# Kernel tuning notes

Measured on AMD Instinct MI355X. Metric: run time of the kernel, lower is better.

The kernel has to match this reference:

```python
import jax, jax.numpy as jnp
import numpy as np

B, T, E = 2, 2048, 2048
H, NOPE, ROPE, VD, KVR, DR = 16, 64, 32, 64, 256, 2
QKD = NOPE + ROPE  # 96
LOWR = KVR // 4    # hypernet low_rank=4 -> 64


def _rope_angles(position, dim):
    # freqs_cis angles: pos * 10000^(-2i/dim), matching torch rotary with theta=10000
    inv = jnp.exp(jnp.arange(0, dim, 2, dtype=jnp.float32) * (-jnp.log(jnp.float32(10000.0)) / dim))
    return position.astype(jnp.float32)[..., None] * inv  # (1, T, dim//2)


def _apply_rotary(x, ang):
    # x: (B,T,H,D); pairs are consecutive elements (view_as_complex semantics)
    x2 = x.reshape(x.shape[:-1] + (-1, 2))
    c = jnp.cos(ang)[:, :, None, :]
    s = jnp.sin(ang)[:, :, None, :]
    xr, xi = x2[..., 0], x2[..., 1]
    return jnp.stack([xr * c - xi * s, xr * s + xi * c], axis=-1).reshape(x.shape)


def _layernorm(x, g, b, eps=1e-5):
    m = jnp.mean(x, axis=-1, keepdims=True)
    v = jnp.var(x, axis=-1, keepdims=True)
    return (x - m) * jax.lax.rsqrt(v + eps) * g + b


def _sinusoid_pe(t, d):
    pos = jnp.arange(t, dtype=jnp.float32)[:, None]
    div = jnp.exp(jnp.arange(0, d, 2, dtype=jnp.float32) * (-jnp.log(jnp.float32(10000.0)) / d))
    pe = jnp.zeros((t, d), dtype=jnp.float32)
    pe = pe.at[:, 0::2].set(jnp.sin(pos * div)).at[:, 1::2].set(jnp.cos(pos * div))
    return pe


def setup_inputs() -> dict:
    key = jax.random.key(0)
    ks = jax.random.split(key, 16)
    sd = 0.02
    return {
        "query": jax.random.normal(ks[0], (B, T, E), jnp.float32),
        "key": jax.random.normal(ks[1], (B, T, E), jnp.float32),
        "value": jax.random.normal(ks[2], (B, T, E), jnp.float32),
        "position": jnp.arange(T, dtype=jnp.int32)[None, :],
        # weights stored transposed for right-multiply (x @ W)
        "wq": jax.random.normal(ks[3], (E, H * QKD), jnp.float32) * sd,
        "wkv_a": jax.random.normal(ks[4], (E, KVR + ROPE), jnp.float32) * sd,
        "kv_gamma": jnp.ones((KVR,), jnp.float32),
        "kv_beta": jnp.zeros((KVR,), jnp.float32),
        # torch layout (H*(NOPE+VD), KVR) kept for faithful view(H,-1,KVR) absorb
        "wkv_b": jax.random.normal(ks[5], (H * (NOPE + VD), KVR), jnp.float32) * sd,
        "wo": jax.random.normal(ks[6], (H * VD, E), jnp.float32) * sd,
        "fc_c_w": jax.random.normal(ks[7], (KVR, LOWR), jnp.float32) * sd,
        "fc_c_b": jnp.zeros((LOWR,), jnp.float32),
        "fc_p_w": jax.random.normal(ks[8], (KVR, LOWR), jnp.float32) * sd,
        "fc_p_b": jnp.zeros((LOWR,), jnp.float32),
    }


def reference(query, key, value, position, wq, wkv_a, kv_gamma, kv_beta, wkv_b, wo,
              fc_c_w, fc_c_b, fc_p_w, fc_p_b):
    bsz, seqlen, _ = query.shape
    # queries: low-rank-free path (q_lora_rank=0)
    q = (query @ wq).reshape(bsz, seqlen, H, QKD)
    q_nope, q_pe = q[..., :NOPE], q[..., NOPE:]
    ang = _rope_angles(position, ROPE)  # (1, T, ROPE//2)
    q_pe = _apply_rotary(q_pe, ang[:, -seqlen:])
    # key/value latent projection
    kv_all = key @ wkv_a  # (B, T, KVR+ROPE)
    kv, k_pe = kv_all[..., :KVR], kv_all[..., KVR:]
    k_pe = _apply_rotary(k_pe[:, :, None, :], ang)[:, :, 0, :]  # (B, T, ROPE)
    kv_norm = _layernorm(kv, kv_gamma, kv_beta)  # (B, T, KVR)
    # hypernetwork temporal downsampling weights (train path, T_input=kv_norm)
    t = -(-seqlen // DR)
    C = jnp.repeat(_sinusoid_pe(t, KVR), DR, axis=0)[:seqlen]  # (T, KVR)
    C2 = C @ fc_c_w + fc_c_b           # (T, LOWR)
    P2 = kv_norm @ fc_p_w + fc_p_b     # (B, T, LOWR)
    W = jax.nn.sigmoid(jnp.einsum('tc,bsc->bts', C2, P2))  # (B, T, T)
    idx = jnp.arange(seqlen)
    chunk = idx // DR
    # chunk mask: cumulative within-chunk causal accumulation
    zero_mask = ((chunk[:, None] == chunk[None, :]) & (idx[None, :] <= idx[:, None])).astype(query.dtype)
    kv_t = jnp.einsum('bts,bsc->btc', W * zero_mask, kv_norm)  # (B, T, KVR)
    # stride-aware causal mask: attend completed chunk-end slots + own in-progress slot
    allowed = (idx[None, :] == idx[:, None]) | ((idx[None, :] < idx[:, None]) & (((idx[None, :] + 1) % DR) == 0))
    attn_mask = jnp.where(allowed, jnp.float32(0.0), jnp.float32(-1e30))
    # absorbed MLA attention
    wb = wkv_b.reshape(H, NOPE + VD, KVR)
    q_abs = jnp.einsum('bshd,hdc->bshc', q_nope, wb[:, :NOPE])  # (B, S, H, KVR)
    scores = (jnp.einsum('bshc,btc->bsht', q_abs, kv_t)
              + jnp.einsum('bshr,btr->bsht', q_pe, k_pe)) * (QKD ** -0.5)
    scores = scores + attn_mask[None, :, None, :]
    attn = jax.nn.softmax(scores, axis=-1)
    x = jnp.einsum('bsht,btc->bshc', attn, kv_t)
    x = jnp.einsum('bshc,hdc->bshd', x, wb[:, NOPE:])  # (B, S, H, VD)
    return x.reshape(bsz, seqlen, H * VD) @ wo
```

## Files before the change

kernel.cpp:

```cpp
#include <hip/hip_runtime.h>
#include <stddef.h>

typedef unsigned short u16;
typedef unsigned short u16x8 __attribute__((ext_vector_type(8)));
typedef short s16x8 __attribute__((ext_vector_type(8)));
typedef float f32x4 __attribute__((ext_vector_type(4)));

#define B_ 2
#define T_ 2048
#define E_ 2048
#define H_ 16

__device__ inline float us2f(u16 u){
  unsigned int i = ((unsigned int)u) << 16;
  return __builtin_bit_cast(float, i);
}
__device__ inline u16 f2us(float f){
  unsigned int x = __builtin_bit_cast(unsigned int, f);
  unsigned int r = (x + 0x7fffu + ((x >> 16) & 1u)) >> 16;
  return (u16)r;
}
__device__ inline f32x4 mfma32(s16x8 a, s16x8 b, f32x4 c){
  return __builtin_amdgcn_mfma_f32_16x16x32_bf16(a, b, c, 0, 0, 0);
}
__device__ inline s16x8 ld8(const u16* p){
  return __builtin_bit_cast(s16x8, *(const u16x8*)p);
}
__device__ inline void gload_lds16(const u16* g, u16* l){
  __builtin_amdgcn_global_load_lds(
      (const __attribute__((address_space(1))) unsigned int*)(g),
      (__attribute__((address_space(3))) unsigned int*)(l), 16, 0, 0);
}

__global__ __launch_bounds__(256) void prep_weights(
    const float* __restrict__ wq, const float* __restrict__ wkva,
    const float* __restrict__ wo, const float* __restrict__ wkvb,
    u16* __restrict__ wqT, u16* __restrict__ wkvaT, u16* __restrict__ woT,
    u16* __restrict__ wkvbB)
{
  __shared__ float tile[32][33];
  const int bid = blockIdx.x;
  const int tid = threadIdx.x;
  if (bid < 5696) {
    const float* in; u16* out; int R, C, bx, by;
    if (bid < 3072)      { in = wq;   out = wqT;   R = 2048; C = 1536; bx = bid % 48;          by = bid / 48; }
    else if (bid < 3648) { in = wkva; out = wkvaT; R = 2048; C = 288;  bx = (bid-3072) % 9;    by = (bid-3072) / 9; }
    else                 { in = wo;   out = woT;   R = 1024; C = 2048; bx = (bid-3648) % 64;   by = (bid-3648) / 64; }
    int tx = tid & 31, ty = tid >> 5;
    int c0 = bx * 32, r0 = by * 32;
    for (int i = ty; i < 32; i += 8){
      int r = r0 + i, c = c0 + tx;
      tile[i][tx] = (r < R && c < C) ? in[(size_t)r * C + c] : 0.f;
    }
    __syncthreads();
    for (int i = ty; i < 32; i += 8){
      int c = c0 + i, r = r0 + tx;
      if (c < C && r < R) out[(size_t)c * R + r] = f2us(tile[tx][i]);
    }
  } else {
    int i = (bid - 5696) * 1024 + tid * 4;
    f32x4 v = *(const f32x4*)(wkvb + i);
    wkvbB[i]   = f2us(v[0]); wkvbB[i+1] = f2us(v[1]);
    wkvbB[i+2] = f2us(v[2]); wkvbB[i+3] = f2us(v[3]);
  }
}

__global__ __launch_bounds__(256) void cvt2_f32_bf16(const float* __restrict__ a,
    const float* __restrict__ b, u16* __restrict__ oa, u16* __restrict__ ob, int n_each)
{
  int idx = (blockIdx.x * 256 + threadIdx.x) * 4;
  const float* in; u16* out; int i;
  if (idx < n_each){ in = a; out = oa; i = idx; }
  else             { in = b; out = ob; i = idx - n_each; }
  if (i + 3 < n_each){
    f32x4 v = *(const f32x4*)(in + i);
    out[i]   = f2us(v[0]); out[i+1] = f2us(v[1]);
    out[i+2] = f2us(v[2]); out[i+3] = f2us(v[3]);
  }
}

template<int A_F32, int OUT_F32>
__global__ __launch_bounds__(256) void gemm_bt(const void* __restrict__ Ap,
    const u16* __restrict__ Bt, void* __restrict__ Cp, int M, int N, int K)
{
  __shared__ __align__(16) u16 As[64][40];
  __shared__ __align__(16) u16 Bs[64][40];
  const int tid  = threadIdx.x;
  const int lane = tid & 63;
  const int wid  = tid >> 6;
  const int quad = lane >> 4;
  const int col  = lane & 15;
  const int bm = blockIdx.y * 64;
  const int bn = blockIdx.x * 64;
  const int lr = tid >> 2;
  const int lc = (tid & 3) * 8;
  const int waveM = wid >> 1, waveN = wid & 1;

  f32x4 acc[2][2];
  for (int i = 0; i < 2; ++i)
    for (int j = 0; j < 2; ++j)
      acc[i][j] = (f32x4){0.f, 0.f, 0.f, 0.f};

  const u16x8 zero8 = {0,0,0,0,0,0,0,0};
  const bool bok = (bn + lr) < N;
  const u16*   arow16 = (const u16*)Ap   + (size_t)(bm + lr) * K + lc;
  const float* arow32 = (const float*)Ap + (size_t)(bm + lr) * K + lc;
  const u16* brow = Bt + (size_t)(bn + lr) * K + lc;

  for (int kk = 0; kk < K; kk += 32) {
    u16x8 av;
    if (A_F32) {
      f32x4 a0 = *(const f32x4*)(arow32 + kk);
      f32x4 a1 = *(const f32x4*)(arow32 + kk + 4);
      av[0]=f2us(a0[0]); av[1]=f2us(a0[1]); av[2]=f2us(a0[2]); av[3]=f2us(a0[3]);
      av[4]=f2us(a1[0]); av[5]=f2us(a1[1]); av[6]=f2us(a1[2]); av[7]=f2us(a1[3]);
    } else {
      av = *(const u16x8*)(arow16 + kk);
    }
    u16x8 bv = bok ? *(const u16x8*)(brow + kk) : zero8;
    __syncthreads();
    *(u16x8*)&As[lr][lc] = av;
    *(u16x8*)&Bs[lr][lc] = bv;
    __syncthreads();
    s16x8 af0 = ld8(&As[waveM*32 + col][quad*8]);
    s16x8 af1 = ld8(&As[waveM*32 + 16 + col][quad*8]);
    s16x8 bf0 = ld8(&Bs[waveN*32 + col][quad*8]);
    s16x8 bf1 = ld8(&Bs[waveN*32 + 16 + col][quad*8]);
    acc[0][0] = mfma32(af0, bf0, acc[0][0]);
    acc[0][1] = mfma32(af0, bf1, acc[0][1]);
    acc[1][0] = mfma32(af1, bf0, acc[1][0]);
    acc[1][1] = mfma32(af1, bf1, acc[1][1]);
  }
  for (int am = 0; am < 2; ++am)
    for (int bnn = 0; bnn < 2; ++bnn)
      for (int i = 0; i < 4; ++i) {
        int r = bm + waveM*32 + am*16 + quad*4 + i;
        int c = bn + waveN*32 + bnn*16 + col;
        if (c < N){
          if (OUT_F32) ((float*)Cp)[(size_t)r * N + c] = acc[am][bnn][i];
          else         ((u16*)Cp)[(size_t)r * N + c]   = f2us(acc[am][bnn][i]);
        }
      }
}

template<int OUT_F32>
__global__ __launch_bounds__(256) void gemm128(const u16* __restrict__ A,
    const u16* __restrict__ Bt, void* __restrict__ Cp, int M, int N, int K, int gx)
{
  __shared__ __align__(16) u16 As[128 * 32];
  __shared__ __align__(16) u16 Bs[128 * 32];
  const int lin = blockIdx.x;
  const int cpx = gridDim.x >> 3;
  const int swz = (lin & 7) * cpx + (lin >> 3);
  const int bxi = swz % gx;
  const int byi = swz / gx;
  const int tid  = threadIdx.x;
  const int lane = tid & 63;
  const int wid  = tid >> 6;
  const int quad = lane >> 4;
  const int col  = lane & 15;
  const int bm = byi * 128;
  const int bn = bxi * 128;
  const int waveM = wid >> 1, waveN = wid & 1;

  const int srow = wid * 16 + (lane >> 2);
  const int scol = (lane & 3) * 8;
  const u16* ga = A  + (size_t)(bm + srow) * K + scol;
  const u16* gb = Bt + (size_t)(bn + srow) * K + scol;
  const size_t rowskip = (size_t)64 * K;
  u16* lAs0 = &As[wid * 512];
  u16* lAs1 = &As[wid * 512 + 2048];
  u16* lBs0 = &Bs[wid * 512];
  u16* lBs1 = &Bs[wid * 512 + 2048];

  f32x4 acc[4][4] = {};

  for (int kk = 0; kk < K; kk += 32) {
    __syncthreads();
    gload_lds16(ga + kk,           lAs0);
    gload_lds16(ga + rowskip + kk, lAs1);
    gload_lds16(gb + kk,           lBs0);
    gload_lds16(gb + rowskip + kk, lBs1);
    __syncthreads();
    s16x8 af[4], bf[4];
#pragma unroll
    for (int i = 0; i < 4; ++i) af[i] = ld8(&As[(waveM*64 + i*16 + col) * 32 + quad*8]);
#pragma unroll
    for (int i = 0; i < 4; ++i) bf[i] = ld8(&Bs[(waveN*64 + i*16 + col) * 32 + quad*8]);
#pragma unroll
    for (int i = 0; i < 4; ++i)
#pragma unroll
      for (int j = 0; j < 4; ++j)
        acc[i][j] = mfma32(af[i], bf[j], acc[i][j]);
  }
#pragma unroll
  for (int i = 0; i < 4; ++i)
#pragma unroll
    for (int j = 0; j < 4; ++j)
#pragma unroll
      for (int r = 0; r < 4; ++r) {
        int row = bm + waveM*64 + i*16 + quad*4 + r;
        int c   = bn + waveN*64 + j*16 + col;
        if (OUT_F32) ((float*)Cp)[(size_t)row * N + c] = acc[i][j][r];
        else         ((u16*)Cp)[(size_t)row * N + c]   = f2us(acc[i][j][r]);
      }
}

__global__ __launch_bounds__(256, 4) void gemm128_sk4(const u16* __restrict__ A,
    const u16* __restrict__ Bt, u16* __restrict__ qp,
    int M, int N, int K, int Klen)
{
  __shared__ __align__(16) u16 As[128 * 32];
  __shared__ __align__(16) u16 Bs[128 * 32];
  const int lin = blockIdx.x;
  const int swz = (lin & 7) * 192 + (lin >> 3);
  const int kh  = swz / 384;
  const int rem = swz % 384;
  const int byi = rem / 12;
  const int bxi = rem % 12;
  const int tid  = threadIdx.x;
  const int lane = tid & 63;
  const int wid  = tid >> 6;
  const int quad = lane >> 4;
  const int col  = lane & 15;
  const int bm = byi * 128;
  const int bn = bxi * 128;
  const int waveM = wid >> 1, waveN = wid & 1;

  const int srow = wid * 16 + (lane >> 2);
  const int scol = (lane & 3) * 8;
  const u16* ga = A  + (size_t)(bm + srow) * K + kh * Klen + scol;
  const u16* gb = Bt + (size_t)(bn + srow) * K + kh * Klen + scol;
  const size_t rowskip = (size_t)64 * K;
  u16* lAs0 = &As[wid * 512];
  u16* lAs1 = &As[wid * 512 + 2048];
  u16* lBs0 = &Bs[wid * 512];
  u16* lBs1 = &Bs[wid * 512 + 2048];
  u16* Cp = qp + (size_t)kh * M * N;

  f32x4 acc[4][4] = {};

  for (int kk = 0; kk < Klen; kk += 32) {
    __syncthreads();
    gload_lds16(ga + kk,           lAs0);
    gload_lds16(ga + rowskip + kk, lAs1);
    gload_lds16(gb + kk,           lBs0);
    gload_lds16(gb + rowskip + kk, lBs1);
    __syncthreads();
    s16x8 af[4], bf[4];
#pragma unroll
    for (int i = 0; i < 4; ++i) af[i] = ld8(&As[(waveM*64 + i*16 + col) * 32 + quad*8]);
#pragma unroll
    for (int i = 0; i < 4; ++i) bf[i] = ld8(&Bs[(waveN*64 + i*16 + col) * 32 + quad*8]);
#pragma unroll
    for (int i = 0; i < 4; ++i)
#pragma unroll
      for (int j = 0; j < 4; ++j)
        acc[i][j] = mfma32(af[i], bf[j], acc[i][j]);
  }
#pragma unroll
  for (int i = 0; i < 4; ++i)
#pragma unroll
    for (int j = 0; j < 4; ++j)
#pragma unroll
      for (int r = 0; r < 4; ++r) {
        int row = bm + waveM*64 + i*16 + quad*4 + r;
        int c   = bn + waveN*64 + j*16 + col;
        Cp[(size_t)row * N + c] = f2us(acc[i][j][r]);
      }
}

__global__ __launch_bounds__(256) void qsplit(const u16* __restrict__ qp,
    const int* __restrict__ pos, u16* __restrict__ qh)
{
  const size_t PS = 4096ull * 1536;
  int idx = blockIdx.x * 256 + threadIdx.x;
  if (idx >= B_*T_*H_*12) return;
  int c    = idx % 12;
  int rest = idx / 12;
  int h    = rest & 15;
  int row  = rest >> 4;
  int t    = row & (T_ - 1);
  int b    = row >> 11;
  size_t off = (size_t)row * 1536 + h * 96 + c * 8;
  u16x8 v0 = *(const u16x8*)(qp + off);
  u16x8 v1 = *(const u16x8*)(qp + PS + off);
  u16x8 v2 = *(const u16x8*)(qp + 2*PS + off);
  u16x8 v3 = *(const u16x8*)(qp + 3*PS + off);
  u16x8 v;
  if (c < 8) {
#pragma unroll
    for (int k = 0; k < 8; ++k)
      v[k] = f2us((us2f(v0[k]) + us2f(v1[k])) + (us2f(v2[k]) + us2f(v3[k])));
  } else {
    int i0 = (c - 8) * 4;
    float pp = (float)pos[t];
#pragma unroll
    for (int k = 0; k < 4; ++k){
      int i = i0 + k;
      float ang = pp * __expf((float)(2*i) * -0.28782313657f);
      float cs = __cosf(ang), sn = __sinf(ang);
      float xr = (us2f(v0[2*k])   + us2f(v1[2*k]))   + (us2f(v2[2*k])   + us2f(v3[2*k]));
      float xi = (us2f(v0[2*k+1]) + us2f(v1[2*k+1])) + (us2f(v2[2*k+1]) + us2f(v3[2*k+1]));
      v[2*k]   = f2us(xr * cs - xi * sn);
      v[2*k+1] = f2us(xr * sn + xi * cs);
    }
  }
  u16* dst = qh + ((size_t)(b * 16 + h) * T_ + t) * 96;
  *(u16x8*)(dst + c * 8) = v;
}

__global__ __launch_bounds__(256) void ln_p2_rope(
    const u16* __restrict__ kvall, const float* __restrict__ gamma,
    const float* __restrict__ beta, const float* __restrict__ fcpw,
    const float* __restrict__ fcpb, const int* __restrict__ pos,
    u16* __restrict__ kvn, float* __restrict__ P2, u16* __restrict__ kpe)
{
  const int row = blockIdx.x;
  if (row >= B_ * T_) return;
  const int tid = threadIdx.x;
  const int lane = tid & 63, wid = tid >> 6;
  __shared__ float kvs[256];
  __shared__ float part[256];
  __shared__ float redS[4], redS2[4];
  const u16* src = kvall + (size_t)row * 288;
  float v = us2f(src[tid]);
  float s1 = v, s2 = v * v;
  for (int off = 1; off < 64; off <<= 1){
    s1 += __shfl_xor(s1, off);
    s2 += __shfl_xor(s2, off);
  }
  if (lane == 0){ redS[wid] = s1; redS2[wid] = s2; }
  __syncthreads();
  float S  = redS[0] + redS[1] + redS[2] + redS[3];
  float Q  = redS2[0] + redS2[1] + redS2[2] + redS2[3];
  float mean = S * (1.f / 256.f);
  float var  = Q * (1.f / 256.f) - mean * mean;
  float rstd = rsqrtf(var + 1e-5f);
  float xn = (v - mean) * rstd * gamma[tid] + beta[tid];
  kvs[tid] = xn;
  kvn[(size_t)row * 256 + tid] = f2us(xn);
  __syncthreads();
  {
    int oc = tid & 63, pp = tid >> 6;
    float acc = 0.f;
#pragma unroll 8
    for (int c = pp * 64; c < pp * 64 + 64; ++c)
      acc += kvs[c] * fcpw[c * 64 + oc];
    part[tid] = acc;
  }
  __syncthreads();
  if (tid < 64) {
    P2[(size_t)row * 64 + tid] = fcpb[tid] + part[tid] + part[64 + tid]
                               + part[128 + tid] + part[192 + tid];
  } else if (tid < 80) {
    int i = tid - 64;
    int t = row & (T_ - 1);
    float ang = (float)pos[t] * __expf((float)(2*i) * -0.28782313657f);
    float c = __cosf(ang), s = __sinf(ang);
    float xr = us2f(src[256 + 2*i]);
    float xi = us2f(src[257 + 2*i]);
    kpe[(size_t)row * 32 + 2*i]     = f2us(xr * c - xi * s);
    kpe[(size_t)row * 32 + 2*i + 1] = f2us(xr * s + xi * c);
  }
}

__global__ __launch_bounds__(256) void c2_kernel(const float* __restrict__ fccw,
    const float* __restrict__ fccb, float* __restrict__ C2)
{
  const int t = blockIdx.x, tid = threadIdx.x;
  __shared__ float pe[256];
  __shared__ float part[256];
  float p = (float)(t >> 1);
  if (tid < 128){
    float div = __expf((float)(2*tid) * -0.03597789207f);
    float a = p * div;
    pe[2*tid]   = __sinf(a);
    pe[2*tid+1] = __cosf(a);
  }
  __syncthreads();
  {
    int oc = tid & 63, pp = tid >> 6;
    float acc = 0.f;
#pragma unroll 8
    for (int c = pp * 64; c < pp * 64 + 64; ++c)
      acc += pe[c] * fccw[c * 64 + oc];
    part[tid] = acc;
  }
  __syncthreads();
  if (tid < 64)
    C2[t * 64 + tid] = fccb[tid] + part[tid] + part[64 + tid]
                     + part[128 + tid] + part[192 + tid];
}

__global__ __launch_bounds__(64) void kvt_kernel(const float* __restrict__ C2,
    const float* __restrict__ P2, const u16* __restrict__ kvn, u16* __restrict__ kvt)
{
  const int row = blockIdx.x;
  if (row >= B_ * T_) return;
  const int lane = threadIdx.x;
  const int t = row & (T_ - 1);
  float c2v = C2[t * 64 + lane];
  float da = c2v * P2[(size_t)row * 64 + lane];
  for (int off = 1; off < 64; off <<= 1) da += __shfl_xor(da, off);
  float wtt = 1.f / (1.f + __expf(-da));
  const bool odd = (t & 1);
  float wts = 0.f;
  if (odd){
    float db = c2v * P2[(size_t)(row - 1) * 64 + lane];
    for (int off = 1; off < 64; off <<= 1) db += __shfl_xor(db, off);
    wts = 1.f / (1.f + __expf(-db));
  }
  for (int c = lane; c < 256; c += 64){
    float val = wtt * us2f(kvn[(size_t)row * 256 + c]);
    if (odd) val += wts * us2f(kvn[(size_t)(row - 1) * 256 + c]);
    kvt[(size_t)row * 256 + c] = f2us(val);
  }
}

__global__ __launch_bounds__(256) void vtkc_kernel(const u16* __restrict__ kvb,
    const u16* __restrict__ kpe, u16* __restrict__ Vt, u16* __restrict__ Kc)
{
  __shared__ __align__(16) u16 tile[64][72];
  const int tid = threadIdx.x;
  if (blockIdx.x < 512) {
    const int bid = blockIdx.x;
    const int jt = bid & 15;
    const int h  = (bid >> 4) & 15;
    const int b  = bid >> 8;
    const int jl = tid >> 2;
    const int dseg = (tid & 3) * 16;
    const int j0 = jt * 64;
    {
      int s_ = 2 * (j0 + jl) + 1;
      const u16* src = kvb + ((size_t)(b * T_ + s_)) * 2048 + h * 128 + 64 + dseg;
      *(u16x8*)&tile[jl][dseg]     = *(const u16x8*)(src);
      *(u16x8*)&tile[jl][dseg + 8] = *(const u16x8*)(src + 8);
    }
    __syncthreads();
    const int dl = tid >> 2;
    const int jseg = (tid & 3) * 16;
    u16* dst = Vt + ((size_t)(b * 16 + h) * 64 + dl) * 1024 + j0 + jseg;
    u16x8 o;
    for (int r = 0; r < 8; ++r) o[r] = tile[jseg + r][dl];
    *(u16x8*)dst = o;
    for (int r = 0; r < 8; ++r) o[r] = tile[jseg + 8 + r][dl];
    *(u16x8*)(dst + 8) = o;
  } else {
    int idx = (blockIdx.x - 512) * 256 + tid;
    int c  = idx % 12;
    int j  = (idx / 12) & 1023;
    int bh = idx / (12 * 1024);
    if (bh >= B_ * H_) return;
    int b = bh >> 4, h = bh & 15;
    int t = 2 * j + 1;
    u16x8 v;
    if (c < 8) v = *(const u16x8*)(kvb + ((size_t)(b * T_ + t)) * 2048 + h * 128 + c * 8);
    else       v = *(const u16x8*)(kpe + ((size_t)(b * T_ + t)) * 32 + (c - 8) * 8);
    int kl = j & 63;
    int cs = (c & 12) | ((c & 3) ^ ((kl >> 1) & 3));
    *(u16x8*)(Kc + ((size_t)bh * 1024 + j) * 96 + cs * 8) = v;
  }
}

__global__ __launch_bounds__(256) void attn_kernel(
    const u16* __restrict__ qh, const u16* __restrict__ kvb,
    const u16* __restrict__ kpe, const u16* __restrict__ Kc,
    const u16* __restrict__ Vt, u16* __restrict__ xout)
{
  __shared__ __align__(16) u16 Ks[64 * 96];
  __shared__ __align__(16) u16 Vs[64][72];
  __shared__ __align__(16) u16 pbufA[4][16 * 72];
  const int tid  = threadIdx.x;
  const int wid  = tid >> 6;
  const int lane = tid & 63;
  const int quad = lane >> 4;
  const int col  = lane & 15;
  const int qt   = 31 - (blockIdx.x >> 5);
  const int bh   = blockIdx.x & 31;
  const int b    = bh >> 4;
  const int h    = bh & 15;
  u16* pbuf = pbufA[wid];
  const float scale = 0.10206207262f;
  const u16* KcH = Kc + (size_t)bh * 1024 * 96;
  const u16* VtH = Vt + (size_t)bh * 64 * 1024;
  const int t0 = qt * 64 + wid * 16;
  const int qo = (quad * 8) ^ (((col >> 1) & 3) << 3);

  s16x8 aq0, aq1, aq2;
  {
    const u16* qrow = qh + ((size_t)bh * T_ + t0 + col) * 96;
    aq0 = ld8(qrow + quad * 8);
    aq1 = ld8(qrow + 32 + quad * 8);
    aq2 = ld8(qrow + 64 + quad * 8);
  }
  float sself;
  {
    const int t = t0 + col;
    const u16* qrow = qh + ((size_t)bh * T_ + t) * 96;
    const u16* ka = kvb + ((size_t)(b * T_ + t)) * 2048 + h * 128;
    const u16* kp = kpe + ((size_t)(b * T_ + t)) * 32;
    float a = 0.f;
#pragma unroll
    for (int c = 0; c < 8; ++c){
      u16x8 qv = *(const u16x8*)(qrow + c * 8);
      u16x8 kv = *(const u16x8*)(ka + c * 8);
#pragma unroll
      for (int jj = 0; jj < 8; ++jj) a += us2f(qv[jj]) * us2f(kv[jj]);
    }
#pragma unroll
    for (int c = 0; c < 4; ++c){
      u16x8 qv = *(const u16x8*)(qrow + 64 + c * 8);
      u16x8 kv = *(const u16x8*)(kp + c * 8);
#pragma unroll
      for (int jj = 0; jj < 8; ++jj) a += us2f(qv[jj]) * us2f(kv[jj]);
    }
    sself = a * scale;
  }
  float es[4], lacc[4];
  f32x4 O[4];
#pragma unroll
  for (int i = 0; i < 4; ++i){
    es[i] = __expf(__shfl(sself, quad * 4 + i));
    lacc[i] = 0.f;
  }
#pragma unroll
  for (int nt = 0; nt < 4; ++nt)
#pragma unroll
    for (int i = 0; i < 4; ++i){
      int t = t0 + quad * 4 + i;
      O[nt][i] = es[i] * us2f(kvb[((size_t)(b * T_ + t)) * 2048 + h * 128 + 64 + nt * 16 + col]);
    }

  const int nb = (qt * 32 + 94) >> 6;
  for (int blk = 0; blk < nb; ++blk) {
    const int jb = blk * 64;
    __syncthreads();
    {
      const u16* gk = KcH + (size_t)jb * 96 + (wid * 3) * 512 + lane * 8;
      u16* lk = &Ks[(wid * 3) * 512];
#pragma unroll
      for (int k = 0; k < 3; ++k)
        gload_lds16(gk + k * 512, lk + k * 512);
      int d = tid >> 2, c4 = tid & 3;
      const u16* gv = VtH + (size_t)d * 1024 + jb + c4 * 16;
      u16* lv = &Vs[d][c4 * 16];
      *(u16x8*)(lv)     = *(const u16x8*)(gv);
      *(u16x8*)(lv + 8) = *(const u16x8*)(gv + 8);
    }
    __syncthreads();
#pragma unroll
    for (int cc = 0; cc < 2; ++cc){
      const u16* k0 = &Ks[(cc * 32 + col) * 96];
      const u16* k1 = k0 + 16 * 96;
      f32x4 s0 = {0,0,0,0}, s1 = {0,0,0,0};
      s0 = mfma32(aq0, ld8(k0 + qo), s0);
      s0 = mfma32(aq1, ld8(k0 + 32 + qo), s0);
      s0 = mfma32(aq2, ld8(k0 + 64 + qo), s0);
      s1 = mfma32(aq0, ld8(k1 + qo), s1);
      s1 = mfma32(aq1, ld8(k1 + 32 + qo), s1);
      s1 = mfma32(aq2, ld8(k1 + 64 + qo), s1);
      int key0 = jb + cc * 32 + col;
#pragma unroll
      for (int i = 0; i < 4; ++i){
        int lim = (t0 + quad * 4 + i) >> 1;
        float p0 = (key0 < lim)      ? __expf(s0[i] * scale) : 0.f;
        float p1 = (key0 + 16 < lim) ? __expf(s1[i] * scale) : 0.f;
        lacc[i] += p0 + p1;
        pbuf[(quad * 4 + i) * 72 + cc * 32 + col]      = f2us(p0);
        pbuf[(quad * 4 + i) * 72 + cc * 32 + 16 + col] = f2us(p1);
      }
    }
    asm volatile("s_waitcnt lgkmcnt(0)" ::: "memory");
    __builtin_amdgcn_sched_barrier(0);
#pragma unroll
    for (int cc = 0; cc < 2; ++cc){
      s16x8 pf = ld8(&pbuf[col * 72 + cc * 32 + quad * 8]);
#pragma unroll
      for (int nt = 0; nt < 4; ++nt)
        O[nt] = mfma32(pf, ld8(&Vs[nt * 16 + col][cc * 32 + quad * 8]), O[nt]);
    }
  }
#pragma unroll
  for (int i = 0; i < 4; ++i){
    float l = lacc[i];
    l += __shfl_xor(l, 1);
    l += __shfl_xor(l, 2);
    l += __shfl_xor(l, 4);
    l += __shfl_xor(l, 8);
    lacc[i] = es[i] + l;
  }
#pragma unroll
  for (int nt = 0; nt < 4; ++nt)
#pragma unroll
    for (int i = 0; i < 4; ++i){
      int t = t0 + quad * 4 + i;
      xout[((size_t)(b * T_ + t)) * 1024 + h * 64 + nt * 16 + col] = f2us(O[nt][i] / lacc[i]);
    }
}

extern "C" void kernel_launch(void* const* d_in, const int* in_sizes, int n_in,
                              void* d_out, int out_size, void* d_ws, size_t ws_size,
                              hipStream_t stream)
{
  (void)in_sizes; (void)n_in; (void)out_size; (void)ws_size;
  const float* query = (const float*)d_in[0];
  const float* key_  = (const float*)d_in[1];
  const int*   pos   = (const int*)d_in[3];
  const float* wq    = (const float*)d_in[4];
  const float* wkva  = (const float*)d_in[5];
  const float* gamma = (const float*)d_in[6];
  const float* beta  = (const float*)d_in[7];
  const float* wkvb  = (const float*)d_in[8];
  const float* wo    = (const float*)d_in[9];
  const float* fccw  = (const float*)d_in[10];
  const float* fccb  = (const float*)d_in[11];
  const float* fcpw  = (const float*)d_in[12];
  const float* fcpb  = (const float*)d_in[13];

  char* p = (char*)d_ws;
  auto alloc = [&](size_t bytes) -> void* {
    void* r = (void*)p;
    p += (bytes + 255) & ~(size_t)255;
    return r;
  };
  u16* wqT    = (u16*)alloc(1536ull * 2048 * 2);
  u16* wkvaT  = (u16*)alloc(288ull  * 2048 * 2);
  u16* woT    = (u16*)alloc(2048ull * 1024 * 2);
  u16* wkvbB  = (u16*)alloc(2048ull * 256 * 2);
  u16* queryB = (u16*)alloc(4096ull * 2048 * 2);
  u16* keyB   = (u16*)alloc(4096ull * 2048 * 2);
  u16* qp     = (u16*)alloc(4ull * 4096 * 1536 * 2);
  u16* qh     = (u16*)alloc(65536ull * 96 * 2);
  u16* kvall  = (u16*)alloc(4096ull * 288 * 2);
  u16* kvn    = (u16*)alloc(4096ull * 256 * 2);
  u16* kpe    = (u16*)alloc(4096ull * 32 * 2);
  float* P2   = (float*)alloc(4096ull * 64 * 4);
  float* C2   = (float*)alloc(2048ull * 64 * 4);
  u16* kvt    = (u16*)alloc(4096ull * 256 * 2);
  u16* kvb    = (u16*)alloc(4096ull * 2048 * 2);
  char* q8 = (char*)qp;
  u16* Kc = (u16*)q8;
  u16* Vt = (u16*)(q8 + ((32ull*1024*96*2 + 255) & ~255ull));
  u16* x  = (u16*)(q8 + ((32ull*1024*96*2 + 255) & ~255ull)
                      + ((2048ull*1024*2   + 255) & ~255ull));

  prep_weights<<<6208, 256, 0, stream>>>(wq, wkva, wo, wkvb, wqT, wkvaT, woT, wkvbB);
  cvt2_f32_bf16<<<16384, 256, 0, stream>>>(query, key_, queryB, keyB, 4096 * 2048);

  gemm128_sk4<<<1536, 256, 0, stream>>>(queryB, wqT, qp, 4096, 1536, 2048, 512);
  gemm_bt<0,0><<<dim3(5, 64), 256, 0, stream>>>(keyB, wkvaT, kvall, 4096, 288, 2048);

  qsplit<<<3072, 256, 0, stream>>>(qp, pos, qh);
  ln_p2_rope<<<4096, 256, 0, stream>>>(kvall, gamma, beta, fcpw, fcpb, pos, kvn, P2, kpe);
  c2_kernel<<<2048, 256, 0, stream>>>(fccw, fccb, C2);
  kvt_kernel<<<4096, 64, 0, stream>>>(C2, P2, kvn, kvt);

  gemm128<0><<<512, 256, 0, stream>>>(kvt, wkvbB, kvb, 4096, 2048, 256, 16);
  vtkc_kernel<<<2048, 256, 0, stream>>>(kvb, kpe, Vt, Kc);
  attn_kernel<<<1024, 256, 0, stream>>>(qh, kvb, kpe, Kc, Vt, x);

  gemm128<1><<<512, 256, 0, stream>>>(x, woT, d_out, 4096, 2048, 1024, 16);
}
```

Measured before the change: 354.6 us.

## Double-buffer LDS in GEMM kernels and halve split-K for Q projection

Both gemm128 and the split-K Q-projection GEMM now use two LDS buffers, so the next K tile's global-to-LDS loads are issued while MFMAs run on the current tile, with one barrier per iteration instead of two. The Q projection also drops from split-K 4 to split-K 2. That halves the partial-sum buffer and the reads in qsplit, at the cost of fewer blocks and longer per-block K loops. Doubling LDS per block and removing the occupancy hint may lower the number of resident blocks.

New measurement: 347.2 us. 2.1% less time.

```diff
diff --git a/kernel.cpp b/kernel.cpp
--- a/kernel.cpp
+++ b/kernel.cpp
@@ -147,8 +147,8 @@
 __global__ __launch_bounds__(256) void gemm128(const u16* __restrict__ A,
     const u16* __restrict__ Bt, void* __restrict__ Cp, int M, int N, int K, int gx)
 {
-  __shared__ __align__(16) u16 As[128 * 32];
-  __shared__ __align__(16) u16 Bs[128 * 32];
+  __shared__ __align__(16) u16 As[2 * 128 * 32];
+  __shared__ __align__(16) u16 Bs[2 * 128 * 32];
   const int lin = blockIdx.x;
   const int cpx = gridDim.x >> 3;
   const int swz = (lin & 7) * cpx + (lin >> 3);
@@ -168,30 +168,45 @@
   const u16* ga = A  + (size_t)(bm + srow) * K + scol;
   const u16* gb = Bt + (size_t)(bn + srow) * K + scol;
   const size_t rowskip = (size_t)64 * K;
-  u16* lAs0 = &As[wid * 512];
-  u16* lAs1 = &As[wid * 512 + 2048];
-  u16* lBs0 = &Bs[wid * 512];
-  u16* lBs1 = &Bs[wid * 512 + 2048];
 
   f32x4 acc[4][4] = {};
-
-  for (int kk = 0; kk < K; kk += 32) {
-    __syncthreads();
-    gload_lds16(ga + kk,           lAs0);
-    gload_lds16(ga + rowskip + kk, lAs1);
-    gload_lds16(gb + kk,           lBs0);
-    gload_lds16(gb + rowskip + kk, lBs1);
-    __syncthreads();
+  const int nt = K >> 5;
+
+  auto STAGE = [&](int buf, int kk){
+    u16* la = &As[buf * 4096 + wid * 512];
+    u16* lb = &Bs[buf * 4096 + wid * 512];
+    gload_lds16(ga + kk,           la);
+    gload_lds16(ga + rowskip + kk, la + 2048);
+    gload_lds16(gb + kk,           lb);
+    gload_lds16(gb + rowskip + kk, lb + 2048);
+  };
+
+  STAGE(0, 0);
+  asm volatile("s_waitcnt vmcnt(0)" ::: "memory");
+  __builtin_amdgcn_s_barrier();
+  __builtin_amdgcn_sched_barrier(0);
+
+  int cur = 0;
+  for (int it = 0; it < nt; ++it){
+    if (it + 1 < nt) STAGE(cur ^ 1, (it + 1) * 32);
+    const u16* as = &As[cur * 4096];
+    const u16* bs = &Bs[cur * 4096];
     s16x8 af[4], bf[4];
 #pragma unroll
-    for (int i = 0; i < 4; ++i) af[i] = ld8(&As[(waveM*64 + i*16 + col) * 32 + quad*8]);
-#pragma unroll
-    for (int i = 0; i < 4; ++i) bf[i] = ld8(&Bs[(waveN*64 + i*16 + col) * 32 + quad*8]);
+    for (int i = 0; i < 4; ++i) af[i] = ld8(&as[(waveM*64 + i*16 + col) * 32 + quad*8]);
+#pragma unroll
+    for (int i = 0; i < 4; ++i) bf[i] = ld8(&bs[(waveN*64 + i*16 + col) * 32 + quad*8]);
 #pragma unroll
     for (int i = 0; i < 4; ++i)
 #pragma unroll
       for (int j = 0; j < 4; ++j)
         acc[i][j] = mfma32(af[i], bf[j], acc[i][j]);
+    asm volatile("s_waitcnt lgkmcnt(0)" ::: "memory");
+    if (it + 1 < nt)
+      asm volatile("s_waitcnt vmcnt(0)" ::: "memory");
+    __builtin_amdgcn_s_barrier();
+    __builtin_amdgcn_sched_barrier(0);
+    cur ^= 1;
   }
 #pragma unroll
   for (int i = 0; i < 4; ++i)
@@ -206,14 +221,14 @@
       }
 }
 
-__global__ __launch_bounds__(256, 4) void gemm128_sk4(const u16* __restrict__ A,
+__global__ __launch_bounds__(256) void gemm128_sk(const u16* __restrict__ A,
     const u16* __restrict__ Bt, u16* __restrict__ qp,
     int M, int N, int K, int Klen)
 {
-  __shared__ __align__(16) u16 As[128 * 32];
-  __shared__ __align__(16) u16 Bs[128 * 32];
+  __shared__ __align__(16) u16 As[2 * 128 * 32];
+  __shared__ __align__(16) u16 Bs[2 * 128 * 32];
   const int lin = blockIdx.x;
-  const int swz = (lin & 7) * 192 + (lin >> 3);
+  const int swz = (lin & 7) * 96 + (lin >> 3);
   const int kh  = swz / 384;
   const int rem = swz % 384;
   const int byi = rem / 12;
@@ -232,31 +247,46 @@
   const u16* ga = A  + (size_t)(bm + srow) * K + kh * Klen + scol;
   const u16* gb = Bt + (size_t)(bn + srow) * K + kh * Klen + scol;
   const size_t rowskip = (size_t)64 * K;
-  u16* lAs0 = &As[wid * 512];
-  u16* lAs1 = &As[wid * 512 + 2048];
-  u16* lBs0 = &Bs[wid * 512];
-  u16* lBs1 = &Bs[wid * 512 + 2048];
   u16* Cp = qp + (size_t)kh * M * N;
 
   f32x4 acc[4][4] = {};
-
-  for (int kk = 0; kk < Klen; kk += 32) {
-    __syncthreads();
-    gload_lds16(ga + kk,           lAs0);
-    gload_lds16(ga + rowskip + kk, lAs1);
-    gload_lds16(gb + kk,           lBs0);
-    gload_lds16(gb + rowskip + kk, lBs1);
-    __syncthreads();
+  const int nt = Klen >> 5;
+
+  auto STAGE = [&](int buf, int kk){
+    u16* la = &As[buf * 4096 + wid * 512];
+    u16* lb = &Bs[buf * 4096 + wid * 512];
+    gload_lds16(ga + kk,           la);
+    gload_lds16(ga + rowskip + kk, la + 2048);
+    gload_lds16(gb + kk,           lb);
+    gload_lds16(gb + rowskip + kk, lb + 2048);
+  };
+
+  STAGE(0, 0);
+  asm volatile("s_waitcnt vmcnt(0)" ::: "memory");
+  __builtin_amdgcn_s_barrier();
+  __builtin_amdgcn_sched_barrier(0);
+
+  int cur = 0;
+  for (int it = 0; it < nt; ++it){
+    if (it + 1 < nt) STAGE(cur ^ 1, (it + 1) * 32);
+    const u16* as = &As[cur * 4096];
+    const u16* bs = &Bs[cur * 4096];
     s16x8 af[4], bf[4];
 #pragma unroll
-    for (int i = 0; i < 4; ++i) af[i] = ld8(&As[(waveM*64 + i*16 + col) * 32 + quad*8]);
-#pragma unroll
-    for (int i = 0; i < 4; ++i) bf[i] = ld8(&Bs[(waveN*64 + i*16 + col) * 32 + quad*8]);
+    for (int i = 0; i < 4; ++i) af[i] = ld8(&as[(waveM*64 + i*16 + col) * 32 + quad*8]);
+#pragma unroll
+    for (int i = 0; i < 4; ++i) bf[i] = ld8(&bs[(waveN*64 + i*16 + col) * 32 + quad*8]);
 #pragma unroll
     for (int i = 0; i < 4; ++i)
 #pragma unroll
       for (int j = 0; j < 4; ++j)
         acc[i][j] = mfma32(af[i], bf[j], acc[i][j]);
+    asm volatile("s_waitcnt lgkmcnt(0)" ::: "memory");
+    if (it + 1 < nt)
+      asm volatile("s_waitcnt vmcnt(0)" ::: "memory");
+    __builtin_amdgcn_s_barrier();
+    __builtin_amdgcn_sched_barrier(0);
+    cur ^= 1;
   }
 #pragma unroll
   for (int i = 0; i < 4; ++i)
@@ -285,13 +315,10 @@
   size_t off = (size_t)row * 1536 + h * 96 + c * 8;
   u16x8 v0 = *(const u16x8*)(qp + off);
   u16x8 v1 = *(const u16x8*)(qp + PS + off);
-  u16x8 v2 = *(const u16x8*)(qp + 2*PS + off);
-  u16x8 v3 = *(const u16x8*)(qp + 3*PS + off);
   u16x8 v;
   if (c < 8) {
 #pragma unroll
-    for (int k = 0; k < 8; ++k)
-      v[k] = f2us((us2f(v0[k]) + us2f(v1[k])) + (us2f(v2[k]) + us2f(v3[k])));
+    for (int k = 0; k < 8; ++k) v[k] = f2us(us2f(v0[k]) + us2f(v1[k]));
   } else {
     int i0 = (c - 8) * 4;
     float pp = (float)pos[t];
@@ -300,8 +327,8 @@
       int i = i0 + k;
       float ang = pp * __expf((float)(2*i) * -0.28782313657f);
       float cs = __cosf(ang), sn = __sinf(ang);
-      float xr = (us2f(v0[2*k])   + us2f(v1[2*k]))   + (us2f(v2[2*k])   + us2f(v3[2*k]));
-      float xi = (us2f(v0[2*k+1]) + us2f(v1[2*k+1])) + (us2f(v2[2*k+1]) + us2f(v3[2*k+1]));
+      float xr = us2f(v0[2*k])   + us2f(v1[2*k]);
+      float xi = us2f(v0[2*k+1]) + us2f(v1[2*k+1]);
       v[2*k]   = f2us(xr * cs - xi * sn);
       v[2*k+1] = f2us(xr * sn + xi * cs);
     }
@@ -630,7 +657,7 @@
   u16* wkvbB  = (u16*)alloc(2048ull * 256 * 2);
   u16* queryB = (u16*)alloc(4096ull * 2048 * 2);
   u16* keyB   = (u16*)alloc(4096ull * 2048 * 2);
-  u16* qp     = (u16*)alloc(4ull * 4096 * 1536 * 2);
+  u16* qp     = (u16*)alloc(2ull * 4096 * 1536 * 2);
   u16* qh     = (u16*)alloc(65536ull * 96 * 2);
   u16* kvall  = (u16*)alloc(4096ull * 288 * 2);
   u16* kvn    = (u16*)alloc(4096ull * 256 * 2);
@@ -648,7 +675,7 @@
   prep_weights<<<6208, 256, 0, stream>>>(wq, wkva, wo, wkvb, wqT, wkvaT, woT, wkvbB);
   cvt2_f32_bf16<<<16384, 256, 0, stream>>>(query, key_, queryB, keyB, 4096 * 2048);
 
-  gemm128_sk4<<<1536, 256, 0, stream>>>(queryB, wqT, qp, 4096, 1536, 2048, 512);
+  gemm128_sk<<<768, 256, 0, stream>>>(queryB, wqT, qp, 4096, 1536, 2048, 1024);
   gemm_bt<0,0><<<dim3(5, 64), 256, 0, stream>>>(keyB, wkvaT, kvall, 4096, 288, 2048);
 
   qsplit<<<3072, 256, 0, stream>>>(qp, pos, qh);
```
